# Performance work log

Hardware: AMD Instinct MI355X
Metric: run time of the kernel (lower is better)

## Reference

```python
import jax, jax.numpy as jnp
import numpy as np

EPS = 1e-5

def _bn_train(x, gamma, beta):
    # BatchNorm2d in training mode: batch stats over (N,H,W), biased variance
    mean = jnp.mean(x, axis=(0, 2, 3), keepdims=True)
    var = jnp.mean((x - mean) ** 2, axis=(0, 2, 3), keepdims=True)
    xn = (x - mean) / jnp.sqrt(var + EPS)
    return xn * gamma[None, :, None, None] + beta[None, :, None, None]

def _bin_act(x):
    # forward: sign(x); backward: grad of clamp(x,-1,1) (STE)
    c = jnp.clip(x, -1.0, 1.0)
    return jax.lax.stop_gradient(jnp.sign(x) - c) + c

def _bin_conv(x, w_flat, out_chn, in_chn, k=3, stride=1, padding=1):
    w = w_flat.reshape(out_chn, in_chn, k, k)
    scale = jax.lax.stop_gradient(jnp.mean(jnp.abs(w), axis=(1, 2, 3), keepdims=True))
    cw = jnp.clip(w, -1.0, 1.0)
    bw = jax.lax.stop_gradient(scale * jnp.sign(w) - cw) + cw
    return jax.lax.conv_general_dilated(
        x, bw, window_strides=(stride, stride),
        padding=[(padding, padding), (padding, padding)],
        dimension_numbers=('NCHW', 'OIHW', 'NCHW'))

def _prelu(x, a):
    return jnp.where(x >= 0, x, a * x)

def setup_inputs() -> dict:
    key = jax.random.key(0)
    ks = jax.random.split(key, 4)
    C = 128
    x = jax.random.normal(ks[0], (64, C, 56, 56), dtype=jnp.float32)
    # HardBinaryConv stores weights as (n,1); init small, mixed-sign
    w1 = (jax.random.uniform(ks[1], (C * C * 9, 1), dtype=jnp.float32) - 0.5) * 0.002
    w2 = (jax.random.uniform(ks[2], (C * C * 9, 1), dtype=jnp.float32) - 0.5) * 0.002
    ones = jnp.ones((C,), jnp.float32)
    zeros = jnp.zeros((C,), jnp.float32)
    a = jnp.float32(0.25)
    return {
        'x': x,
        'bn1_g': ones, 'bn1_b': zeros,
        'w1': w1, 'prelu1_a': a,
        'bn2_g': ones, 'bn2_b': zeros,
        'w2': w2, 'prelu2_a': a,
        'bn3_g': ones, 'bn3_b': zeros,
        'prelu3_a': a,
    }

def reference(x, bn1_g, bn1_b, w1, prelu1_a, bn2_g, bn2_b, w2, prelu2_a, bn3_g, bn3_b, prelu3_a):
    C = x.shape[1]
    out = _bn_train(x, bn1_g, bn1_b)
    out = _bin_act(out)
    out = _prelu(_bin_conv(out, w1, C, C), prelu1_a)
    out = _bn_train(out, bn2_g, bn2_b)
    out = _bin_act(out)
    out = _bin_conv(out, w2, C, C)
    out = _prelu(out, prelu2_a)
    out = _bn_train(out, bn3_g, bn3_b)
    out = out + x  # identity shortcut (stride=1, in_planes==planes)
    out = _prelu(out, prelu3_a)
    return out
```

## Files before the change

### kernel.cpp

```cpp
#include <hip/hip_runtime.h>
#include <hip/hip_bf16.h>

typedef __attribute__((ext_vector_type(8))) short short8;
typedef __attribute__((ext_vector_type(4))) int i32x4;

#define HW     3136
#define M_TOT  200704
#define NSTEP  18
#define NBLK   896
#define SLABB  44544

__device__ __forceinline__ void gload_lds16(const void* g, void* l) {
    __builtin_amdgcn_global_load_lds(
        (const __attribute__((address_space(1))) void*)g,
        (__attribute__((address_space(3))) void*)l, 16, 0, 0);
}

__global__ __launch_bounds__(256) void wsign_kernel(const float* __restrict__ w1,
                                                    const float* __restrict__ w2,
                                                    char* __restrict__ ws1,
                                                    char* __restrict__ ws2) {
    int i = blockIdx.x * 256 + threadIdx.x;
    const float* w = w1;
    char* wsz = ws1;
    if (i >= 147456) { i -= 147456; w = w2; wsz = ws2; }
    int e = i & 15, l = (i >> 4) & 63, f = (i >> 10) & 7, s = i >> 13;
    int cout = f * 16 + (l & 15);
    int k = s * 64 + (l >> 4) * 16 + e;
    int tap = k >> 7, cin = k & 127;
    float v = w[(cout * 128 + cin) * 9 + tap];
    wsz[i] = v > 0.f ? (char)1 : (v < 0.f ? (char)-1 : (char)0);
}

__global__ __launch_bounds__(256) void wscale_kernel(const float* __restrict__ w1,
                                                     const float* __restrict__ w2,
                                                     float* __restrict__ scale1,
                                                     float* __restrict__ scale2) {
    int o = blockIdx.x;
    const float* w = w1;
    float* scale = scale1;
    if (o >= 128) { o -= 128; w = w2; scale = scale2; }
    int t = threadIdx.x;
    float s = 0.f;
    for (int i = t; i < 1152; i += 256) s += fabsf(w[o * 1152 + i]);
    __shared__ float r1[256];
    r1[t] = s; __syncthreads();
    for (int off = 128; off > 0; off >>= 1) {
        if (t < off) r1[t] += r1[t + off];
        __syncthreads();
    }
    if (t == 0) scale[o] = r1[0] * (1.f / 1152.f);
}

__global__ __launch_bounds__(256) void stats_nchw_kernel(const float* __restrict__ x,
                                                         float* __restrict__ psum,
                                                         float* __restrict__ psq) {
    int bid = blockIdx.x;
    int n = bid >> 7, c = bid & 127;
    const float* p = x + (n * 128 + c) * HW;
    int t = threadIdx.x;
    float s = 0.f, q = 0.f;
    for (int i = t; i < HW; i += 256) { float v = p[i]; s += v; q += v * v; }
    __shared__ float r1[256], r2[256];
    r1[t] = s; r2[t] = q; __syncthreads();
    for (int off = 128; off > 0; off >>= 1) {
        if (t < off) { r1[t] += r1[t + off]; r2[t] += r2[t + off]; }
        __syncthreads();
    }
    if (t == 0) { psum[c * 64 + n] = r1[0]; psq[c * 64 + n] = r2[0]; }
}

__global__ void finalize_kernel(const float* __restrict__ psum, const float* __restrict__ psq,
                                int P, float* __restrict__ mean, float* __restrict__ rstd) {
    int c = threadIdx.x;
    if (c >= 128) return;
    float s = 0.f, q = 0.f;
    for (int j = 0; j < P; ++j) { s += psum[c * P + j]; q += psq[c * P + j]; }
    const float invN = 1.f / 200704.f;
    float m = s * invN;
    float var = q * invN - m * m;
    mean[c] = m;
    rstd[c] = 1.f / sqrtf(var + 1e-5f);
}

__global__ __launch_bounds__(256) void finalizeB_kernel(const float* __restrict__ psumB,
                                                        const float* __restrict__ psqB,
                                                        float* __restrict__ mean,
                                                        float* __restrict__ rstd) {
    int c = blockIdx.x, t = threadIdx.x;
    float s = 0.f, q = 0.f;
    for (int j = t; j < NBLK; j += 256) { s += psumB[j * 128 + c]; q += psqB[j * 128 + c]; }
    __shared__ float r1[256], r2[256];
    r1[t] = s; r2[t] = q; __syncthreads();
    for (int off = 128; off > 0; off >>= 1) {
        if (t < off) { r1[t] += r1[t + off]; r2[t] += r2[t + off]; }
        __syncthreads();
    }
    if (t == 0) {
        const float invN = 1.f / 200704.f;
        float m = r1[0] * invN;
        float var = r2[0] * invN - m * m;
        mean[c] = m;
        rstd[c] = 1.f / sqrtf(var + 1e-5f);
    }
}

__global__ __launch_bounds__(256) void act1_kernel(const float* __restrict__ x,
        const float* __restrict__ mean, const float* __restrict__ rstd,
        const float* __restrict__ g, const float* __restrict__ b,
        char* __restrict__ apad) {
    __shared__ float row[128 * 57];
    int blk = blockIdx.x;
    int n = blk / 58, hp = blk - n * 58;
    char* o = apad + (n * 58 + hp) * 58 * 128;
    int t = threadIdx.x;
    if (hp == 0 || hp == 57) {
        for (int i4 = t; i4 < 58 * 32; i4 += 256)
            *(char4*)(o + i4 * 4) = make_char4(0, 0, 0, 0);
        return;
    }
    const float* src = x + n * (128 * HW) + (hp - 1) * 56;
    for (int i = t; i < 128 * 56; i += 256) {
        int c = i / 56, w = i - c * 56;
        row[c * 57 + w] = src[c * HW + w];
    }
    __syncthreads();
    for (int i4 = t; i4 < 58 * 32; i4 += 256) {
        int wp = i4 >> 5;
        int c0 = (i4 & 31) * 4;
        char q[4] = {0, 0, 0, 0};
        if (wp >= 1 && wp <= 56) {
#pragma unroll
            for (int k = 0; k < 4; ++k) {
                int c = c0 + k;
                float xn = (row[c * 57 + wp - 1] - mean[c]) * rstd[c] * g[c] + b[c];
                q[k] = xn > 0.f ? 1 : (xn < 0.f ? -1 : 0);
            }
        }
        *(char4*)(o + wp * 128 + c0) = make_char4(q[0], q[1], q[2], q[3]);
    }
}

__global__ __launch_bounds__(256) void act2_kernel(const short* __restrict__ p1,
        const float* __restrict__ scale1, const float* __restrict__ a1ptr,
        const float* __restrict__ mean, const float* __restrict__ rstd,
        const float* __restrict__ g, const float* __restrict__ b,
        char* __restrict__ apad) {
    __shared__ float row[128 * 57];
    int blk = blockIdx.x;
    int n = blk / 58, hp = blk - n * 58;
    char* o = apad + (n * 58 + hp) * 58 * 128;
    int t = threadIdx.x;
    if (hp == 0 || hp == 57) {
        for (int i4 = t; i4 < 58 * 32; i4 += 256)
            *(char4*)(o + i4 * 4) = make_char4(0, 0, 0, 0);
        return;
    }
    float a1 = a1ptr[0];
    const short* src = p1 + n * HW + (hp - 1) * 56;
    for (int i = t; i < 128 * 56; i += 256) {
        int c = i / 56, w = i - c * 56;
        float v = scale1[c] * (float)src[(size_t)c * M_TOT + w];
        row[c * 57 + w] = v >= 0.f ? v : a1 * v;
    }
    __syncthreads();
    for (int i4 = t; i4 < 58 * 32; i4 += 256) {
        int wp = i4 >> 5;
        int c0 = (i4 & 31) * 4;
        char q[4] = {0, 0, 0, 0};
        if (wp >= 1 && wp <= 56) {
#pragma unroll
            for (int k = 0; k < 4; ++k) {
                int c = c0 + k;
                float xn = (row[c * 57 + wp - 1] - mean[c]) * rstd[c] * g[c] + b[c];
                q[k] = xn > 0.f ? 1 : (xn < 0.f ? -1 : 0);
            }
        }
        *(char4*)(o + wp * 128 + c0) = make_char4(q[0], q[1], q[2], q[3]);
    }
}

__global__ __launch_bounds__(256, 2) void conv_kernel(
        const char* __restrict__ apad,
        const char* __restrict__ wswz,
        const float* __restrict__ scale,
        const float* __restrict__ aptr,
        short* __restrict__ obuf,
        float* __restrict__ psumB,
        float* __restrict__ psqB) {
    __shared__ __align__(1024) char lds[SLABB + 3 * 8192];

    const int tid = threadIdx.x;
    const int lane = tid & 63;
    const int wid = tid >> 6;
    const int l15 = lane & 15;
    const int lq = lane >> 4;
    const int wr = wid >> 1;
    const int wc = wid & 1;

    int bid = blockIdx.x;
    int mblk = (bid & 7) * 112 + (bid >> 3);
    const int n = mblk / 14;
    const int hg = mblk - n * 14;
    const int m0 = n * HW + hg * 224;

    const char* slabsrc = apad + (size_t)(n * 58 + hg * 4) * 58 * 128;
    char* slab = lds;
    char* Abuf = lds + SLABB;

    {
#pragma unroll
        for (int i = 0; i < 11; ++i) {
            int gbyte = i * 4096 + tid * 16;
            if (i < 10 || gbyte < SLABB) {
                int r = gbyte >> 7;
                int cp = (gbyte >> 4) & 7;
                int wp = r % 58;
                gload_lds16(slabsrc + (gbyte & ~127) + ((cp ^ (wp & 7)) << 4),
                            slab + i * 4096 + wid * 1024);
            }
        }
    }

    int Pm[7], Wm[7];
#pragma unroll
    for (int mi = 0; mi < 7; ++mi) {
        int mloc = wc * 112 + mi * 16 + l15;
        int ho = mloc / 56;
        int w = mloc - ho * 56;
        Pm[mi] = (ho * 58 + w) * 128;
        Wm[mi] = w;
    }

    auto stageA = [&](int s, int buf) {
        const char* wsrc = wswz + s * 8192 + tid * 16;
        gload_lds16(wsrc,        Abuf + buf * 8192 + wid * 1024);
        gload_lds16(wsrc + 4096, Abuf + buf * 8192 + 4096 + wid * 1024);
    };

    i32x4 acc[4][7];
#pragma unroll
    for (int i = 0; i < 4; ++i)
#pragma unroll
        for (int j = 0; j < 7; ++j)
            acc[i][j] = (i32x4){0, 0, 0, 0};

    stageA(0, 0);
    stageA(1, 1);

    for (int s = 0; s < NSTEP; ++s) {
        if (s + 1 < NSTEP) asm volatile("s_waitcnt vmcnt(2)" ::: "memory");
        else               asm volatile("s_waitcnt vmcnt(0)" ::: "memory");
        __builtin_amdgcn_s_barrier();
        __builtin_amdgcn_sched_barrier(0);
        if (s + 2 < NSTEP) stageA(s + 2, (s + 2) % 3);

        int tap = s >> 1;
        int dh = tap / 3;
        int dw = tap - dh * 3;
        int Q = (dh * 58 + dw) * 128;
        int s4 = (s & 1) * 4;
        int c16 = s4 + lq;

        const char* abuf = Abuf + (s % 3) * 8192;
        i32x4 af[4], bf[7];
#pragma unroll
        for (int ci = 0; ci < 4; ++ci)
            af[ci] = *(const i32x4*)(abuf + (wr * 4 + ci) * 1024 + lane * 16);
#pragma unroll
        for (int mi = 0; mi < 7; ++mi) {
            int wxd = (Wm[mi] + dw) & 7;
            bf[mi] = *(const i32x4*)(slab + Pm[mi] + Q + ((c16 ^ wxd) << 4));
        }
#pragma unroll
        for (int ci = 0; ci < 4; ++ci)
#pragma unroll
            for (int mi = 0; mi < 7; ++mi)
                acc[ci][mi] = __builtin_amdgcn_mfma_i32_16x16x64_i8(
                    af[ci], bf[mi], acc[ci][mi], 0, 0, 0);
    }

    float alpha = aptr[0];
    float* partS = (float*)Abuf;
    float* partQ = (float*)(Abuf + 1024);
#pragma unroll
    for (int ci = 0; ci < 4; ++ci) {
        int cb = wr * 64 + ci * 16 + lq * 4;
#pragma unroll
        for (int r = 0; r < 4; ++r) {
            float sc = scale[cb + r];
            short* op = obuf + (size_t)(cb + r) * M_TOT + m0 + wc * 112 + l15;
            float s = 0.f, q = 0.f;
#pragma unroll
            for (int mi = 0; mi < 7; ++mi) {
                int iv = acc[ci][mi][r];
                float v = (float)iv * sc;
                float pv = v >= 0.f ? v : alpha * v;
                op[mi * 16] = (short)iv;
                s += pv; q += pv * pv;
            }
#pragma unroll
            for (int msk = 1; msk <= 8; msk <<= 1) {
                s += __shfl_xor(s, msk, 64);
                q += __shfl_xor(q, msk, 64);
            }
            if (l15 == 0) { partS[wc * 128 + cb + r] = s; partQ[wc * 128 + cb + r] = q; }
        }
    }
    __syncthreads();
    if (tid < 128) {
        psumB[bid * 128 + tid] = partS[tid] + partS[128 + tid];
        psqB [bid * 128 + tid] = partQ[tid] + partQ[128 + tid];
    }
}

__global__ __launch_bounds__(256) void final_kernel(const short* __restrict__ p2,
        const float* __restrict__ scale2, const float* __restrict__ a2ptr,
        const float* __restrict__ x,
        const float* __restrict__ mean, const float* __restrict__ rstd,
        const float* __restrict__ g, const float* __restrict__ b,
        const float* __restrict__ a3ptr, float* __restrict__ out) {
    int bid = blockIdx.x;
    int n = bid >> 7, c = bid & 127;
    float sc = scale2[c], a2 = a2ptr[0];
    float m = mean[c], r = rstd[c], gg = g[c], bb = b[c], a3 = a3ptr[0];
    const short* pp = p2 + (size_t)c * M_TOT + n * HW;
    const float* xx = x + (n * 128 + c) * HW;
    float* oo = out + (n * 128 + c) * HW;
    int t = threadIdx.x;
    for (int i8 = t; i8 < 392; i8 += 256) {
        short8 v = *(const short8*)(pp + i8 * 8);
        float4 x0 = *(const float4*)(xx + i8 * 8);
        float4 x1 = *(const float4*)(xx + i8 * 8 + 4);
        float o[8];
#pragma unroll
        for (int k = 0; k < 8; ++k) {
            float pv = (float)v[k] * sc;
            pv = pv >= 0.f ? pv : a2 * pv;
            float xv = (k < 4) ? ((const float*)&x0)[k] : ((const float*)&x1)[k - 4];
            float val = (pv - m) * r * gg + bb + xv;
            o[k] = val >= 0.f ? val : a3 * val;
        }
        *(float4*)(oo + i8 * 8)     = make_float4(o[0], o[1], o[2], o[3]);
        *(float4*)(oo + i8 * 8 + 4) = make_float4(o[4], o[5], o[6], o[7]);
    }
}

extern "C" void kernel_launch(void* const* d_in, const int* in_sizes, int n_in,
                              void* d_out, int out_size, void* d_ws, size_t ws_size,
                              hipStream_t stream) {
    const float* x  = (const float*)d_in[0];
    const float* g1 = (const float*)d_in[1];
    const float* b1 = (const float*)d_in[2];
    const float* w1 = (const float*)d_in[3];
    const float* a1 = (const float*)d_in[4];
    const float* g2 = (const float*)d_in[5];
    const float* b2 = (const float*)d_in[6];
    const float* w2 = (const float*)d_in[7];
    const float* a2 = (const float*)d_in[8];
    const float* g3 = (const float*)d_in[9];
    const float* b3 = (const float*)d_in[10];
    const float* a3 = (const float*)d_in[11];
    float* out = (float*)d_out;
    char* ws = (char*)d_ws;

    float* scale1 = (float*)(ws);
    float* scale2 = (float*)(ws + 512);
    float* mean1  = (float*)(ws + 1024);
    float* rstd1  = (float*)(ws + 1536);
    float* mean2  = (float*)(ws + 2048);
    float* rstd2  = (float*)(ws + 2560);
    float* mean3  = (float*)(ws + 3072);
    float* rstd3  = (float*)(ws + 3584);
    float* psum   = (float*)(ws + 4096);
    float* psq    = (float*)(ws + 36864);
    float* psumB  = (float*)(ws + 69632);
    float* psqB   = (float*)(ws + 872448);
    char* wswz1   = (char*)(ws + 1675264);
    char* wswz2   = (char*)(ws + 1822720);
    char* apad8   = (char*)(ws + 1970176);
    short* buf2s  = (short*)(ws + 29528064);
    short* buf1s  = (short*)out;

    wscale_kernel<<<256, 256, 0, stream>>>(w1, w2, scale1, scale2);
    wsign_kernel<<<1152, 256, 0, stream>>>(w1, w2, wswz1, wswz2);

    stats_nchw_kernel<<<8192, 256, 0, stream>>>(x, psum, psq);
    finalize_kernel<<<1, 128, 0, stream>>>(psum, psq, 64, mean1, rstd1);
    act1_kernel<<<3712, 256, 0, stream>>>(x, mean1, rstd1, g1, b1, apad8);
    conv_kernel<<<NBLK, 256, 0, stream>>>(apad8, wswz1, scale1, a1, buf1s, psumB, psqB);

    finalizeB_kernel<<<128, 256, 0, stream>>>(psumB, psqB, mean2, rstd2);
    act2_kernel<<<3712, 256, 0, stream>>>(buf1s, scale1, a1, mean2, rstd2, g2, b2, apad8);
    conv_kernel<<<NBLK, 256, 0, stream>>>(apad8, wswz2, scale2, a2, buf2s, psumB, psqB);

    finalizeB_kernel<<<128, 256, 0, stream>>>(psumB, psqB, mean3, rstd3);
    final_kernel<<<8192, 256, 0, stream>>>(buf2s, scale2, a2, x, mean3, rstd3, g3, b3, a3, out);
}
```

Before: 247.4 us.

## Restructure conv weight pipeline to per-tap double buffering and vectorize activation loads

The int8 conv main loop now stages a full tap of weights (16KB) per iteration into two LDS buffers, replacing 18 half-tap steps with a three-deep buffer. This halves the number of barriers and waitcnt points, and s_setprio raises wave priority around the MFMA bursts. The act1 and act2 kernels now load input rows with float4 and short8 vector reads instead of scalar reads. In exchange, LDS use rises slightly and the wait before each tap drains every outstanding load (vmcnt(0)), so the weight prefetch has less slack. Partial sums are moved to the second buffer so they do not collide.

```diff
diff --git a/kernel.cpp b/kernel.cpp
--- a/kernel.cpp
+++ b/kernel.cpp
@@ -6,7 +6,7 @@
 
 #define HW     3136
 #define M_TOT  200704
-#define NSTEP  18
+#define NTAP   9
 #define NBLK   896
 #define SLABB  44544
 
@@ -120,9 +120,13 @@
         return;
     }
     const float* src = x + n * (128 * HW) + (hp - 1) * 56;
-    for (int i = t; i < 128 * 56; i += 256) {
-        int c = i / 56, w = i - c * 56;
-        row[c * 57 + w] = src[c * HW + w];
+    for (int i4 = t; i4 < 128 * 14; i4 += 256) {
+        int c = i4 / 14, w4 = (i4 - c * 14) * 4;
+        float4 v = *(const float4*)(src + c * HW + w4);
+        row[c * 57 + w4 + 0] = v.x;
+        row[c * 57 + w4 + 1] = v.y;
+        row[c * 57 + w4 + 2] = v.z;
+        row[c * 57 + w4 + 3] = v.w;
     }
     __syncthreads();
     for (int i4 = t; i4 < 58 * 32; i4 += 256) {
@@ -158,10 +162,15 @@
     }
     float a1 = a1ptr[0];
     const short* src = p1 + n * HW + (hp - 1) * 56;
-    for (int i = t; i < 128 * 56; i += 256) {
-        int c = i / 56, w = i - c * 56;
-        float v = scale1[c] * (float)src[(size_t)c * M_TOT + w];
-        row[c * 57 + w] = v >= 0.f ? v : a1 * v;
+    for (int i8 = t; i8 < 128 * 7; i8 += 256) {
+        int c = i8 / 7, w8 = (i8 - c * 7) * 8;
+        short8 v = *(const short8*)(src + (size_t)c * M_TOT + w8);
+        float sc = scale1[c];
+#pragma unroll
+        for (int k = 0; k < 8; ++k) {
+            float val = sc * (float)v[k];
+            row[c * 57 + w8 + k] = val >= 0.f ? val : a1 * val;
+        }
     }
     __syncthreads();
     for (int i4 = t; i4 < 58 * 32; i4 += 256) {
@@ -188,7 +197,7 @@
         short* __restrict__ obuf,
         float* __restrict__ psumB,
         float* __restrict__ psqB) {
-    __shared__ __align__(1024) char lds[SLABB + 3 * 8192];
+    __shared__ __align__(1024) char lds[SLABB + 2 * 16384];
 
     const int tid = threadIdx.x;
     const int lane = tid & 63;
@@ -232,10 +241,12 @@
         Wm[mi] = w;
     }
 
-    auto stageA = [&](int s, int buf) {
-        const char* wsrc = wswz + s * 8192 + tid * 16;
-        gload_lds16(wsrc,        Abuf + buf * 8192 + wid * 1024);
-        gload_lds16(wsrc + 4096, Abuf + buf * 8192 + 4096 + wid * 1024);
+    auto stageA = [&](int t, int buf) {
+        const char* wsrc = wswz + t * 16384 + tid * 16;
+        char* dst = Abuf + buf * 16384 + wid * 1024;
+#pragma unroll
+        for (int i = 0; i < 4; ++i)
+            gload_lds16(wsrc + i * 4096, dst + i * 4096);
     };
 
     i32x4 acc[4][7];
@@ -246,43 +257,44 @@
             acc[i][j] = (i32x4){0, 0, 0, 0};
 
     stageA(0, 0);
-    stageA(1, 1);
-
-    for (int s = 0; s < NSTEP; ++s) {
-        if (s + 1 < NSTEP) asm volatile("s_waitcnt vmcnt(2)" ::: "memory");
-        else               asm volatile("s_waitcnt vmcnt(0)" ::: "memory");
+
+    for (int t = 0; t < NTAP; ++t) {
+        asm volatile("s_waitcnt vmcnt(0)" ::: "memory");
         __builtin_amdgcn_s_barrier();
         __builtin_amdgcn_sched_barrier(0);
-        if (s + 2 < NSTEP) stageA(s + 2, (s + 2) % 3);
-
-        int tap = s >> 1;
-        int dh = tap / 3;
-        int dw = tap - dh * 3;
+        if (t + 1 < NTAP) stageA(t + 1, (t + 1) & 1);
+
+        int dh = t / 3;
+        int dw = t - dh * 3;
         int Q = (dh * 58 + dw) * 128;
-        int s4 = (s & 1) * 4;
-        int c16 = s4 + lq;
-
-        const char* abuf = Abuf + (s % 3) * 8192;
-        i32x4 af[4], bf[7];
-#pragma unroll
-        for (int ci = 0; ci < 4; ++ci)
-            af[ci] = *(const i32x4*)(abuf + (wr * 4 + ci) * 1024 + lane * 16);
-#pragma unroll
-        for (int mi = 0; mi < 7; ++mi) {
-            int wxd = (Wm[mi] + dw) & 7;
-            bf[mi] = *(const i32x4*)(slab + Pm[mi] + Q + ((c16 ^ wxd) << 4));
-        }
-#pragma unroll
-        for (int ci = 0; ci < 4; ++ci)
-#pragma unroll
-            for (int mi = 0; mi < 7; ++mi)
-                acc[ci][mi] = __builtin_amdgcn_mfma_i32_16x16x64_i8(
-                    af[ci], bf[mi], acc[ci][mi], 0, 0, 0);
+        const char* abuf = Abuf + (t & 1) * 16384;
+
+#pragma unroll
+        for (int ks = 0; ks < 2; ++ks) {
+            i32x4 af[4], bf[7];
+#pragma unroll
+            for (int ci = 0; ci < 4; ++ci)
+                af[ci] = *(const i32x4*)(abuf + ks * 8192 + (wr * 4 + ci) * 1024 + lane * 16);
+            int c16 = ks * 4 + lq;
+#pragma unroll
+            for (int mi = 0; mi < 7; ++mi) {
+                int wxd = (Wm[mi] + dw) & 7;
+                bf[mi] = *(const i32x4*)(slab + Pm[mi] + Q + ((c16 ^ wxd) << 4));
+            }
+            __builtin_amdgcn_s_setprio(1);
+#pragma unroll
+            for (int ci = 0; ci < 4; ++ci)
+#pragma unroll
+                for (int mi = 0; mi < 7; ++mi)
+                    acc[ci][mi] = __builtin_amdgcn_mfma_i32_16x16x64_i8(
+                        af[ci], bf[mi], acc[ci][mi], 0, 0, 0);
+            __builtin_amdgcn_s_setprio(0);
+        }
     }
 
     float alpha = aptr[0];
-    float* partS = (float*)Abuf;
-    float* partQ = (float*)(Abuf + 1024);
+    float* partS = (float*)(Abuf + 16384);
+    float* partQ = (float*)(Abuf + 16384 + 1024);
 #pragma unroll
     for (int ci = 0; ci < 4; ++ci) {
         int cb = wr * 64 + ci * 16 + lq * 4;
```

Result: no change. 244.8 us (-1.0%).
